# Kernel optimization log

Measured on AMD Instinct MI355X. Metric: run time of the kernel, lower is better.

## Reference

```python
import jax, jax.numpy as jnp
import numpy as np

N_NODES = 50000
N_EDGES = 800000
IN_FEATS = 9
H_FEATS = 64
HEADS = 3
N_CLASSES = 2
NEG_SLOPE = 0.2  # DGL GATConv default leaky_relu slope


def _gat_layer(x, src, dst, W, attn_l, attn_r, bias, n_nodes):
    """One DGL-style GATConv: returns [N, H, F_out] (pre head-sum)."""
    H, Fo = attn_l.shape
    feat = (x @ W).reshape(n_nodes, H, Fo)            # [N,H,Fo]
    el = jnp.einsum('nhf,hf->nh', feat, attn_l)        # [N,H]
    er = jnp.einsum('nhf,hf->nh', feat, attn_r)        # [N,H]
    e = jax.nn.leaky_relu(el[src] + er[dst], negative_slope=NEG_SLOPE)  # [E,H]
    # edge softmax over incoming edges per destination node
    m = jax.ops.segment_max(e, dst, num_segments=n_nodes)               # [N,H]
    ex = jnp.exp(e - m[dst])                                             # [E,H]
    s = jax.ops.segment_sum(ex, dst, num_segments=n_nodes)              # [N,H]
    alpha = ex / s[dst]                                                  # [E,H]
    # attention-weighted neighbor aggregation
    rst = jax.ops.segment_sum(alpha[:, :, None] * feat[src], dst,
                              num_segments=n_nodes)                      # [N,H,Fo]
    return rst + bias.reshape(1, H, Fo)


def setup_inputs() -> dict:
    key = jax.random.key(0)
    ks = jax.random.split(key, 16)
    feats = jax.random.normal(ks[0], (N_NODES, IN_FEATS), dtype=jnp.float32)
    src = jax.random.randint(ks[1], (N_EDGES,), 0, N_NODES, dtype=jnp.int32)
    dst = jax.random.randint(ks[2], (N_EDGES,), 0, N_NODES, dtype=jnp.int32)
    sc = 0.1
    # layer 1: in_feats -> H*H_FEATS
    W1 = jax.random.normal(ks[3], (IN_FEATS, HEADS * H_FEATS), dtype=jnp.float32) * sc
    al1 = jax.random.normal(ks[4], (HEADS, H_FEATS), dtype=jnp.float32) * sc
    ar1 = jax.random.normal(ks[5], (HEADS, H_FEATS), dtype=jnp.float32) * sc
    b1 = jnp.zeros((HEADS * H_FEATS,), dtype=jnp.float32)
    # middle block layer: H_FEATS -> H*H_FEATS
    W2 = jax.random.normal(ks[6], (H_FEATS, HEADS * H_FEATS), dtype=jnp.float32) * sc
    al2 = jax.random.normal(ks[7], (HEADS, H_FEATS), dtype=jnp.float32) * sc
    ar2 = jax.random.normal(ks[8], (HEADS, H_FEATS), dtype=jnp.float32) * sc
    b2 = jnp.zeros((HEADS * H_FEATS,), dtype=jnp.float32)
    # output layer: H_FEATS -> H*N_CLASSES
    W3 = jax.random.normal(ks[9], (H_FEATS, HEADS * N_CLASSES), dtype=jnp.float32) * sc
    al3 = jax.random.normal(ks[10], (HEADS, N_CLASSES), dtype=jnp.float32) * sc
    ar3 = jax.random.normal(ks[11], (HEADS, N_CLASSES), dtype=jnp.float32) * sc
    b3 = jnp.zeros((HEADS * N_CLASSES,), dtype=jnp.float32)
    return {"feats": feats, "src": src, "dst": dst,
            "W1": W1, "al1": al1, "ar1": ar1, "b1": b1,
            "W2": W2, "al2": al2, "ar2": ar2, "b2": b2,
            "W3": W3, "al3": al3, "ar3": ar3, "b3": b3}


def reference(feats, src, dst, W1, al1, ar1, b1, W2, al2, ar2, b2, W3, al3, ar3, b3):
    # dropout layers are identity at inference (in_dropout/feat_drop skipped)
    h = _gat_layer(feats, src, dst, W1, al1, ar1, b1, N_NODES).sum(axis=1)  # [N,H_FEATS]
    h = _gat_layer(h, src, dst, W2, al2, ar2, b2, N_NODES).sum(axis=1)       # [N,H_FEATS]
    o = _gat_layer(h, src, dst, W3, al3, ar3, b3, N_NODES).sum(axis=1)       # [N,N_CLASSES]
    return o
```

## Files before the change

### kernel.cpp

```cpp
#include <hip/hip_runtime.h>
#include <hip/hip_fp16.h>

#define N_NODES 50000
#define N_EDGES 800000
#define NBKT 196
#define EPB_BIN 4096
#define NB_BIN ((N_EDGES + EPB_BIN - 1) / EPB_BIN)
#define NB_EL 196
#define NB_PW 48

typedef _Float16 half8 __attribute__((ext_vector_type(8)));
typedef float f32x4 __attribute__((ext_vector_type(4)));

static __device__ __forceinline__ float lrelu(float x) { return fmaxf(x, 0.2f * x); }

static __device__ __forceinline__ float2 h2f(float bits) {
    union { float f; __half2 h; } u;
    u.f = bits;
    return __half22float2(u.h);
}
static __device__ __forceinline__ float f2h2(float a, float b) {
    union { float f; __half2 h; } u;
    u.h = __floats2half2_rn(a, b);
    return u.f;
}

__global__ void __launch_bounds__(256) k_front(const int* __restrict__ dst,
                                               int* __restrict__ bcnt,
                                               const float* __restrict__ x,
                                               const float* __restrict__ W1,
                                               const float* __restrict__ al1,
                                               const float* __restrict__ ar1,
                                               float* __restrict__ xph,
                                               float* __restrict__ er,
                                               const float* __restrict__ W2,
                                               __half* __restrict__ Wt16,
                                               const float* __restrict__ al2,
                                               const float* __restrict__ ar2,
                                               float* __restrict__ Wa2,
                                               float* __restrict__ Wr2) {
    __shared__ int lcnt[NBKT];
    __shared__ float sWa[9 * 3];
    __shared__ float sWr[9 * 3];
    const int t = threadIdx.x;
    const int b = blockIdx.x;

    if (b < NB_BIN) {
        const int e0 = b * EPB_BIN;
        for (int i = t; i < NBKT; i += 256) lcnt[i] = 0;
        __syncthreads();
#pragma unroll
        for (int i = 0; i < 16; ++i) {
            const int e = e0 + i * 256 + t;
            if (e < N_EDGES) atomicAdd(&lcnt[dst[e] >> 8], 1);
        }
        __syncthreads();
        for (int i = t; i < NBKT; i += 256)
            if (lcnt[i]) atomicAdd(&bcnt[i], lcnt[i]);
        return;
    }
    if (b < NB_BIN + NB_EL) {
        if (t < 27) {
            const int h = t / 9, k = t % 9;
            float sa = 0.f, sr = 0.f;
            for (int f = 0; f < 64; ++f) {
                const float w = W1[k * 192 + h * 64 + f];
                sa += w * al1[h * 64 + f];
                sr += w * ar1[h * 64 + f];
            }
            sWa[k * 3 + h] = sa;
            sWr[k * 3 + h] = sr;
        }
        __syncthreads();
        const int n = (b - NB_BIN) * 256 + t;
        if (n >= N_NODES) return;
        const float* __restrict__ xr = x + (size_t)n * 9;
        float xv[9];
        float a0 = 0.f, a1 = 0.f, a2 = 0.f, r0 = 0.f, r1 = 0.f, r2 = 0.f;
#pragma unroll
        for (int k = 0; k < 9; ++k) {
            xv[k] = xr[k];
            a0 += xv[k] * sWa[k * 3 + 0];
            a1 += xv[k] * sWa[k * 3 + 1];
            a2 += xv[k] * sWa[k * 3 + 2];
            r0 += xv[k] * sWr[k * 3 + 0];
            r1 += xv[k] * sWr[k * 3 + 1];
            r2 += xv[k] * sWr[k * 3 + 2];
        }
        float* __restrict__ xo = xph + (size_t)n * 8;
        *reinterpret_cast<float4*>(xo) = make_float4(a0, a1, a2, f2h2(xv[0], xv[1]));
        *reinterpret_cast<float4*>(xo + 4) =
            make_float4(f2h2(xv[2], xv[3]), f2h2(xv[4], xv[5]),
                        f2h2(xv[6], xv[7]), f2h2(xv[8], 0.f));
        *reinterpret_cast<float4*>(er + (size_t)n * 4) = make_float4(r0, r1, r2, 0.f);
        return;
    }
    if (b < NB_BIN + NB_EL + NB_PW) {
        const int idx = (b - (NB_BIN + NB_EL)) * 256 + t;
        if (idx < 64 * 192) {
            const int n = idx / 192, ke = idx % 192;
            Wt16[idx] = __float2half(W2[(ke & 63) * 192 + (ke >> 6) * 64 + n]);
        }
        return;
    }
    if (t < 192) {
        const int h = t >> 6, k = t & 63;
        float sa = 0.f, sr = 0.f;
        for (int f = 0; f < 64; ++f) {
            const float w = W2[k * 192 + h * 64 + f];
            sa += w * al2[h * 64 + f];
            sr += w * ar2[h * 64 + f];
        }
        Wa2[k * 4 + h] = sa;
        Wr2[k * 4 + h] = sr;
        if (h == 0) { Wa2[k * 4 + 3] = 0.f; Wr2[k * 4 + 3] = 0.f; }
    }
}

__global__ void __launch_bounds__(256) k_bin(const int* __restrict__ src,
                                             const int* __restrict__ dst,
                                             const int* __restrict__ bcnt,
                                             int* __restrict__ bfill,
                                             unsigned int* __restrict__ stage) {
    __shared__ int lcnt[NBKT];
    __shared__ int gb[NBKT];
    __shared__ int lf[NBKT];
    __shared__ int sscan[256];
    __shared__ int sbase[256];
    const int t = threadIdx.x;
    const int e0 = blockIdx.x * EPB_BIN;
    const int bv = (t < NBKT) ? bcnt[t] : 0;
    sscan[t] = bv;
    if (t < NBKT) lcnt[t] = 0;
    __syncthreads();
    for (int off = 1; off < 256; off <<= 1) {
        const int u = (t >= off) ? sscan[t - off] : 0;
        __syncthreads();
        sscan[t] += u;
        __syncthreads();
    }
    sbase[t] = sscan[t] - bv;
    int dcache[16];
#pragma unroll
    for (int i = 0; i < 16; ++i) {
        const int e = e0 + i * 256 + t;
        if (e < N_EDGES) {
            const int d = dst[e];
            dcache[i] = d;
            atomicAdd(&lcnt[d >> 8], 1);
        } else dcache[i] = -1;
    }
    __syncthreads();
    for (int i = t; i < NBKT; i += 256) {
        gb[i] = sbase[i] + atomicAdd(&bfill[i], lcnt[i]);
        lf[i] = 0;
    }
    __syncthreads();
#pragma unroll
    for (int i = 0; i < 16; ++i) {
        const int e = e0 + i * 256 + t;
        if (e < N_EDGES) {
            const int d = dcache[i];
            const int bk = d >> 8;
            const int r = atomicAdd(&lf[bk], 1);
            stage[gb[bk] + r] = (unsigned int)src[e] | ((unsigned int)(d & 255) << 16);
        }
    }
}

__global__ void __launch_bounds__(256) k_bscatter2(const unsigned int* __restrict__ stage,
                                                   const int* __restrict__ bcnt,
                                                   int* __restrict__ rowp,
                                                   int* __restrict__ col) {
    __shared__ int lcnt[256];
    __shared__ int lpos[256];
    __shared__ int sexc[256];
    __shared__ int sscan[256];
    const int t = threadIdx.x;
    const int b = blockIdx.x;
    const int n0 = b << 8;
    const int bv = (t < NBKT) ? bcnt[t] : 0;
    sscan[t] = bv;
    lcnt[t] = 0;
    __syncthreads();
    for (int off = 1; off < 256; off <<= 1) {
        const int u = (t >= off) ? sscan[t - off] : 0;
        __syncthreads();
        sscan[t] += u;
        __syncthreads();
    }
    const int base = (b == 0) ? 0 : sscan[b - 1];
    const int end = sscan[b];

    for (int j = base + t; j < end; j += 256)
        atomicAdd(&lcnt[(stage[j] >> 16) & 255], 1);
    __syncthreads();
    const int v = lcnt[t];
    lpos[t] = v;
    __syncthreads();
    for (int off = 1; off < 256; off <<= 1) {
        const int u = (t >= off) ? lpos[t - off] : 0;
        __syncthreads();
        lpos[t] += u;
        __syncthreads();
    }
    sexc[t] = lpos[t] - v;
    if (n0 + t < N_NODES) rowp[n0 + t] = base + sexc[t];
    if (b == NBKT - 1 && t == 0) rowp[N_NODES] = N_EDGES;
    lcnt[t] = 0;
    __syncthreads();
    for (int j = base + t; j < end; j += 256) {
        const unsigned int e = stage[j];
        const int local = (int)(e >> 16) & 255;
        const int r = atomicAdd(&lcnt[local], 1);
        col[base + sexc[local] + r] = (int)(e & 0xFFFFu);
    }
}

__global__ void __launch_bounds__(256, 6) k_l1(const float* __restrict__ xph,
                                               const float* __restrict__ er_in,
                                               const int* __restrict__ rowp,
                                               const int* __restrict__ col,
                                               const float* __restrict__ W1,
                                               const float* __restrict__ b1,
                                               const float* __restrict__ Wa2,
                                               const float* __restrict__ Wr2,
                                               __half* __restrict__ hout,
                                               float* __restrict__ el,
                                               float* __restrict__ er_out) {
    __shared__ union {
        float At[16 * 28];
        float vbuf[16][72];
    } u;
    __shared__ float part[3][16][64];
    const int t = threadIdx.x;
    const int wv = t >> 6;
    const int lane = t & 63;
    const int q = lane >> 4;
    const int ql = lane & 15;
    const int li = wv * 4 + q;
    const int nbase = blockIdx.x * 16;
    const int n = nbase + li;

    {
        const int jb = rowp[n], je = rowp[n + 1];
        const float4 er4 = *reinterpret_cast<const float4*>(er_in + (size_t)n * 4);
        float acc[27];
#pragma unroll
        for (int j = 0; j < 27; ++j) acc[j] = 0.f;
        float sw0 = 0.f, sw1 = 0.f, sw2 = 0.f;

        for (int e = jb + ql; e < je; e += 32) {
            const int e2 = e + 16;
            const bool v2 = (e2 < je);
            const int s1 = col[e];
            const int s2 = v2 ? col[e2] : s1;
            const float* __restrict__ r1 = xph + (size_t)s1 * 8;
            const float* __restrict__ r2 = xph + (size_t)s2 * 8;
            const float4 xa1 = *reinterpret_cast<const float4*>(r1);
            const float4 xb1 = *reinterpret_cast<const float4*>(r1 + 4);
            const float4 xa2 = *reinterpret_cast<const float4*>(r2);
            const float4 xb2 = *reinterpret_cast<const float4*>(r2 + 4);
            const float m2 = v2 ? 1.f : 0.f;
            const float w10 = __expf(lrelu(xa1.x + er4.x));
            const float w11 = __expf(lrelu(xa1.y + er4.y));
            const float w12 = __expf(lrelu(xa1.z + er4.z));
            const float w20 = __expf(lrelu(xa2.x + er4.x)) * m2;
            const float w21 = __expf(lrelu(xa2.y + er4.y)) * m2;
            const float w22 = __expf(lrelu(xa2.z + er4.z)) * m2;
            sw0 += w10 + w20; sw1 += w11 + w21; sw2 += w12 + w22;
            const float2 p10 = h2f(xa1.w), p11 = h2f(xb1.x), p12 = h2f(xb1.y),
                         p13 = h2f(xb1.z), p14 = h2f(xb1.w);
            const float2 p20 = h2f(xa2.w), p21 = h2f(xb2.x), p22 = h2f(xb2.y),
                         p23 = h2f(xb2.z), p24 = h2f(xb2.w);
            const float x1[9] = {p10.x, p10.y, p11.x, p11.y, p12.x, p12.y, p13.x, p13.y, p14.x};
            const float x2[9] = {p20.x, p20.y, p21.x, p21.y, p22.x, p22.y, p23.x, p23.y, p24.x};
#pragma unroll
            for (int k = 0; k < 9; ++k) {
                acc[0 + k]  += w10 * x1[k] + w20 * x2[k];
                acc[9 + k]  += w11 * x1[k] + w21 * x2[k];
                acc[18 + k] += w12 * x1[k] + w22 * x2[k];
            }
        }
#pragma unroll
        for (int off = 1; off < 16; off <<= 1) {
            sw0 += __shfl_xor(sw0, off);
            sw1 += __shfl_xor(sw1, off);
            sw2 += __shfl_xor(sw2, off);
#pragma unroll
            for (int j = 0; j < 27; ++j) acc[j] += __shfl_xor(acc[j], off);
        }
        if (ql == 0) {
            const bool has = (je > jb);
            const float i0 = has ? 1.f / sw0 : 0.f;
            const float i1 = has ? 1.f / sw1 : 0.f;
            const float i2 = has ? 1.f / sw2 : 0.f;
            float* __restrict__ ao = u.At + li * 28;
#pragma unroll
            for (int k = 0; k < 9; ++k) {
                ao[k] = acc[k] * i0;
                ao[9 + k] = acc[9 + k] * i1;
                ao[18 + k] = acc[18 + k] * i2;
            }
        }
    }
    __syncthreads();

    {
        const int h = wv;
        const int c = lane;
        if (h < 3) {
            float wreg[9];
#pragma unroll
            for (int k = 0; k < 9; ++k) wreg[k] = W1[k * 192 + h * 64 + c];
#pragma unroll
            for (int i = 0; i < 16; ++i) {
                const float* __restrict__ arp = u.At + i * 28 + h * 9;
                float acc = 0.f;
#pragma unroll
                for (int k = 0; k < 9; ++k) acc += arp[k] * wreg[k];
                part[h][i][c] = acc;
            }
        }
        __syncthreads();
        const float bsum = b1[c] + b1[64 + c] + b1[128 + c];
        for (int idx = t; idx < 1024; idx += 256) {
            const int i = idx >> 6, cc = idx & 63;
            const float v = part[0][i][cc] + part[1][i][cc] + part[2][i][cc] + bsum;
            hout[(size_t)(nbase + i) * 64 + cc] = __float2half(v);
            u.vbuf[i][cc] = v;
        }
        __syncthreads();
        if (t < 96) {
            const int i = t / 6, r = t % 6;
            const int h3 = (r < 3) ? r : r - 3;
            const float* __restrict__ tab = (r < 3) ? Wa2 : Wr2;
            float s = 0.f;
#pragma unroll 8
            for (int c2 = 0; c2 < 64; ++c2) s += u.vbuf[i][c2] * tab[c2 * 4 + h3];
            if (r < 3) el[(size_t)(nbase + i) * 4 + h3] = s;
            else       er_out[(size_t)(nbase + i) * 4 + h3] = s;
        }
    }
}

__global__ void __launch_bounds__(256, 8) k_aggw64(const __half* __restrict__ x,
                                                   const float* __restrict__ el,
                                                   const float* __restrict__ er,
                                                   const int* __restrict__ rowp,
                                                   const int* __restrict__ col,
                                                   __half* __restrict__ agg) {
    const int wv = threadIdx.x >> 6;
    const int lane = threadIdx.x & 63;
    const int n = blockIdx.x * 4 + wv;
    const int jb = rowp[n], je = rowp[n + 1];

    __shared__ float wbuf[4][3][68];
    __shared__ int cbuf[4][68];
    const float4 er4 = *reinterpret_cast<const float4*>(er + (size_t)n * 4);
    const int p = lane >> 5;
    const int f0 = (lane & 31) * 2;
    float a00 = 0.f, a01 = 0.f, a02 = 0.f;
    float a10 = 0.f, a11 = 0.f, a12 = 0.f;
    float sw0 = 0.f, sw1 = 0.f, sw2 = 0.f;

    for (int c0 = jb; c0 < je; c0 += 64) {
        const int cnt = min(64, je - c0);
        float w0 = 0.f, w1 = 0.f, w2 = 0.f;
        if (lane < cnt) {
            const int s = col[c0 + lane];
            cbuf[wv][lane] = s;
            const float4 e4 = *reinterpret_cast<const float4*>(el + (size_t)s * 4);
            w0 = __expf(lrelu(e4.x + er4.x));
            w1 = __expf(lrelu(e4.y + er4.y));
            w2 = __expf(lrelu(e4.z + er4.z));
            wbuf[wv][0][lane] = w0;
            wbuf[wv][1][lane] = w1;
            wbuf[wv][2][lane] = w2;
        }
        sw0 += w0; sw1 += w1; sw2 += w2;
        int e = 0;
        for (; e + 2 <= cnt; e += 2) {
            const int ei = e + p;
            const int s = cbuf[wv][ei];
            const float2 xv = __half22float2(
                *reinterpret_cast<const __half2*>(x + (size_t)s * 64 + f0));
            const float we0 = wbuf[wv][0][ei];
            const float we1 = wbuf[wv][1][ei];
            const float we2 = wbuf[wv][2][ei];
            a00 += we0 * xv.x; a01 += we1 * xv.x; a02 += we2 * xv.x;
            a10 += we0 * xv.y; a11 += we1 * xv.y; a12 += we2 * xv.y;
        }
        if (e < cnt && p == 0) {
            const int s = cbuf[wv][e];
            const float2 xv = __half22float2(
                *reinterpret_cast<const __half2*>(x + (size_t)s * 64 + f0));
            const float we0 = wbuf[wv][0][e];
            const float we1 = wbuf[wv][1][e];
            const float we2 = wbuf[wv][2][e];
            a00 += we0 * xv.x; a01 += we1 * xv.x; a02 += we2 * xv.x;
            a10 += we0 * xv.y; a11 += we1 * xv.y; a12 += we2 * xv.y;
        }
    }
    a00 += __shfl_xor(a00, 32); a01 += __shfl_xor(a01, 32); a02 += __shfl_xor(a02, 32);
    a10 += __shfl_xor(a10, 32); a11 += __shfl_xor(a11, 32); a12 += __shfl_xor(a12, 32);
#pragma unroll
    for (int off = 32; off > 0; off >>= 1) {
        sw0 += __shfl_xor(sw0, off);
        sw1 += __shfl_xor(sw1, off);
        sw2 += __shfl_xor(sw2, off);
    }
    if (lane < 32) {
        __half* __restrict__ ao = agg + (size_t)n * 192;
        if (je > jb) {
            const float i0 = 1.f / sw0, i1 = 1.f / sw1, i2 = 1.f / sw2;
            *reinterpret_cast<__half2*>(ao + f0) = __floats2half2_rn(a00 * i0, a10 * i0);
            *reinterpret_cast<__half2*>(ao + 64 + f0) = __floats2half2_rn(a01 * i1, a11 * i1);
            *reinterpret_cast<__half2*>(ao + 128 + f0) = __floats2half2_rn(a02 * i2, a12 * i2);
        } else {
            const __half2 z = __floats2half2_rn(0.f, 0.f);
            *reinterpret_cast<__half2*>(ao + f0) = z;
            *reinterpret_cast<__half2*>(ao + 64 + f0) = z;
            *reinterpret_cast<__half2*>(ao + 128 + f0) = z;
        }
    }
}

__global__ void __launch_bounds__(256) k_l23(const __half* __restrict__ aggH,
                                             const __half* __restrict__ Wt,
                                             const float* __restrict__ b2,
                                             const float* __restrict__ W3,
                                             const float* __restrict__ al3,
                                             const float* __restrict__ ar3,
                                             float* __restrict__ feat3p,
                                             float* __restrict__ er3) {
    __shared__ float xl[64 * 68];
    __shared__ float Wl[64 * 6];
    __shared__ float Wal[64 * 3];
    __shared__ float Wrl[64 * 3];
    const int t = threadIdx.x;
    const int n0 = blockIdx.x * 64;
    const int nvalid = min(64, N_NODES - n0);

    {
        const int wv = t >> 6;
        const int lane = t & 63;
        const int quad = lane >> 4;
        const int t16 = lane & 15;
        const int nwave = n0 + wv * 16;
        const int arow = min(nwave + t16, N_NODES - 1);
        half8 a[6];
#pragma unroll
        for (int kb = 0; kb < 6; ++kb)
            a[kb] = *reinterpret_cast<const half8*>(aggH + (size_t)arow * 192 + kb * 32 + quad * 8);
#pragma unroll
        for (int nt = 0; nt < 4; ++nt) {
            const int c = nt * 16 + t16;
            const float bs = b2[c] + b2[64 + c] + b2[128 + c];
            const __half* __restrict__ bt = Wt + (size_t)c * 192 + quad * 8;
            f32x4 acc = {0.f, 0.f, 0.f, 0.f};
#pragma unroll
            for (int kb = 0; kb < 6; ++kb) {
                const half8 bfr = *reinterpret_cast<const half8*>(bt + kb * 32);
                acc = __builtin_amdgcn_mfma_f32_16x16x32_f16(a[kb], bfr, acc, 0, 0, 0);
            }
#pragma unroll
            for (int r = 0; r < 4; ++r)
                xl[(wv * 16 + quad * 4 + r) * 68 + c] = acc[r] + bs;
        }
    }
    for (int idx = t; idx < 384; idx += 256) Wl[idx] = W3[idx];
    if (t < 192) {
        const int k = t & 63, h = t >> 6;
        Wal[k * 3 + h] = W3[k * 6 + h * 2] * al3[h * 2] + W3[k * 6 + h * 2 + 1] * al3[h * 2 + 1];
        Wrl[k * 3 + h] = W3[k * 6 + h * 2] * ar3[h * 2] + W3[k * 6 + h * 2 + 1] * ar3[h * 2 + 1];
    }
    __syncthreads();

#pragma unroll
    for (int hp = 0; hp < 2; ++hp) {
        const int i = (t >> 3) + hp * 32;
        const int slot = t & 7;
        if (i < nvalid && slot < 6) {
            float acc = 0.f;
#pragma unroll
            for (int k4 = 0; k4 < 16; ++k4) {
                const float4 xv = *reinterpret_cast<const float4*>(&xl[i * 68 + 4 * k4]);
                acc += Wl[(4 * k4 + 0) * 6 + slot] * xv.x;
                acc += Wl[(4 * k4 + 1) * 6 + slot] * xv.y;
                acc += Wl[(4 * k4 + 2) * 6 + slot] * xv.z;
                acc += Wl[(4 * k4 + 3) * 6 + slot] * xv.w;
            }
            reinterpret_cast<__half*>(feat3p + (size_t)(n0 + i) * 8)[6 + slot] = __float2half(acc);
        }
        if (t < 192) {
            const int ii = t / 6 + hp * 32, ss = t % 6;
            if (ii < nvalid) {
                const int hh = (ss < 3) ? ss : ss - 3;
                const float* __restrict__ wt = (ss < 3) ? Wal : Wrl;
                float acc = 0.f;
#pragma unroll 4
                for (int k = 0; k < 64; ++k) acc += xl[ii * 68 + k] * wt[k * 3 + hh];
                if (ss < 3) feat3p[(size_t)(n0 + ii) * 8 + hh] = acc;
                else        er3[(size_t)(n0 + ii) * 4 + hh] = acc;
            }
        }
    }
}

__global__ void __launch_bounds__(256, 8) k_agg3(const float* __restrict__ feat3p,
                                                 const float* __restrict__ er3,
                                                 const float* __restrict__ b3,
                                                 const int* __restrict__ rowp,
                                                 const int* __restrict__ col,
                                                 float* __restrict__ out) {
    const int tid = threadIdx.x;
    const int wv = tid >> 6;
    const int lane = tid & 63;
    const int q = lane >> 4;
    const int ql = lane & 15;
    const int n = (blockIdx.x * 4 + wv) * 4 + q;
    const int jb = rowp[n], je = rowp[n + 1];
    const float4 er4 = *reinterpret_cast<const float4*>(er3 + (size_t)n * 4);

    float acc[6];
#pragma unroll
    for (int j = 0; j < 6; ++j) acc[j] = 0.f;
    float sw0 = 0.f, sw1 = 0.f, sw2 = 0.f;

    for (int e = jb + ql; e < je; e += 32) {
        const int e2 = e + 16;
        const bool v2 = (e2 < je);
        const int s1 = col[e];
        const int s2 = v2 ? col[e2] : s1;
        const float* __restrict__ r1 = feat3p + (size_t)s1 * 8;
        const float* __restrict__ r2 = feat3p + (size_t)s2 * 8;
        const float4 fa1 = *reinterpret_cast<const float4*>(r1);
        const float2 fb1 = *reinterpret_cast<const float2*>(r1 + 4);
        const float4 fa2 = *reinterpret_cast<const float4*>(r2);
        const float2 fb2 = *reinterpret_cast<const float2*>(r2 + 4);
        const float m2 = v2 ? 1.f : 0.f;
        const float w10 = __expf(lrelu(fa1.x + er4.x));
        const float w11 = __expf(lrelu(fa1.y + er4.y));
        const float w12 = __expf(lrelu(fa1.z + er4.z));
        const float w20 = __expf(lrelu(fa2.x + er4.x)) * m2;
        const float w21 = __expf(lrelu(fa2.y + er4.y)) * m2;
        const float w22 = __expf(lrelu(fa2.z + er4.z)) * m2;
        sw0 += w10 + w20; sw1 += w11 + w21; sw2 += w12 + w22;
        const float2 f01a = h2f(fa1.w), f23a = h2f(fb1.x), f45a = h2f(fb1.y);
        const float2 f01b = h2f(fa2.w), f23b = h2f(fb2.x), f45b = h2f(fb2.y);
        acc[0] += w10 * f01a.x + w20 * f01b.x;
        acc[1] += w10 * f01a.y + w20 * f01b.y;
        acc[2] += w11 * f23a.x + w21 * f23b.x;
        acc[3] += w11 * f23a.y + w21 * f23b.y;
        acc[4] += w12 * f45a.x + w22 * f45b.x;
        acc[5] += w12 * f45a.y + w22 * f45b.y;
    }
#pragma unroll
    for (int off = 1; off < 16; off <<= 1) {
        sw0 += __shfl_xor(sw0, off);
        sw1 += __shfl_xor(sw1, off);
        sw2 += __shfl_xor(sw2, off);
#pragma unroll
        for (int j = 0; j < 6; ++j) acc[j] += __shfl_xor(acc[j], off);
    }
    if (ql == 0) {
        const bool has = (je > jb);
        const float i0 = has ? 1.f / sw0 : 0.f;
        const float i1 = has ? 1.f / sw1 : 0.f;
        const float i2 = has ? 1.f / sw2 : 0.f;
        const float o0 = acc[0] * i0 + acc[2] * i1 + acc[4] * i2 + b3[0] + b3[2] + b3[4];
        const float o1 = acc[1] * i0 + acc[3] * i1 + acc[5] * i2 + b3[1] + b3[3] + b3[5];
        *reinterpret_cast<float2*>(out + (size_t)n * 2) = make_float2(o0, o1);
    }
}

extern "C" void kernel_launch(void* const* d_in, const int* in_sizes, int n_in,
                              void* d_out, int out_size, void* d_ws, size_t ws_size,
                              hipStream_t stream) {
    const float* feats = (const float*)d_in[0];
    const int* src = (const int*)d_in[1];
    const int* dst = (const int*)d_in[2];
    const float* W1 = (const float*)d_in[3];
    const float* al1 = (const float*)d_in[4];
    const float* ar1 = (const float*)d_in[5];
    const float* b1 = (const float*)d_in[6];
    const float* W2 = (const float*)d_in[7];
    const float* al2 = (const float*)d_in[8];
    const float* ar2 = (const float*)d_in[9];
    const float* b2 = (const float*)d_in[10];
    const float* W3 = (const float*)d_in[11];
    const float* al3 = (const float*)d_in[12];
    const float* ar3 = (const float*)d_in[13];
    const float* b3 = (const float*)d_in[14];
    float* out = (float*)d_out;

    char* ws = (char*)d_ws;
    size_t off = 0;
    auto alloc = [&](size_t bytes) {
        void* p = ws + off;
        off += (bytes + 255) & ~(size_t)255;
        return p;
    };
    __half* aggH = (__half*)alloc((size_t)N_NODES * 192 * 2);
    __half* hbufH = (__half*)alloc((size_t)N_NODES * 64 * 2);
    float* xph = (float*)alloc((size_t)N_NODES * 8 * 4);
    float* el = (float*)alloc((size_t)N_NODES * 4 * 4);
    float* er = (float*)alloc((size_t)N_NODES * 4 * 4);
    int* bcnt = (int*)alloc(512 * 4);
    int* bfill = bcnt + 256;
    int* rowp = (int*)alloc((size_t)(N_NODES + 1) * 4);
    int* col = (int*)alloc((size_t)N_EDGES * 4);
    unsigned int* stage = (unsigned int*)alloc((size_t)N_EDGES * 4);
    __half* Wt16 = (__half*)alloc((size_t)64 * 192 * 2);
    float* Wa2 = (float*)alloc(256 * 4);
    float* Wr2 = (float*)alloc(256 * 4);
    float* feat3p = (float*)alloc((size_t)N_NODES * 8 * 4);
    (void)ws_size;

    const int ab = N_NODES / 4;
    const int qb = N_NODES / 16;
    const int lb = (N_NODES + 63) / 64;

    hipMemsetAsync(bcnt, 0, 512 * 4, stream);
    k_front<<<NB_BIN + NB_EL + NB_PW + 1, 256, 0, stream>>>(
        dst, bcnt, feats, W1, al1, ar1, xph, er, W2, Wt16, al2, ar2, Wa2, Wr2);
    k_bin<<<NB_BIN, 256, 0, stream>>>(src, dst, bcnt, bfill, stage);
    k_bscatter2<<<NBKT, 256, 0, stream>>>(stage, bcnt, rowp, col);

    k_l1<<<qb, 256, 0, stream>>>(xph, er, rowp, col, W1, b1, Wa2, Wr2, hbufH, el, er);

    k_aggw64<<<ab, 256, 0, stream>>>(hbufH, el, er, rowp, col, aggH);

    k_l23<<<lb, 256, 0, stream>>>(aggH, Wt16, b2, W3, al3, ar3, feat3p, er);

    k_agg3<<<qb, 256, 0, stream>>>(feat3p, er, b3, rowp, col, out);
}
```

Baseline: 225.1 us.

## Build CSR with per-node atomic counts and unroll aggregation loops

Replaces the two-pass bucket staging CSR build with per-node degree counting in the front kernel, a per-bucket scan kernel, and a direct atomic scatter of source indices into col. This drops the staging buffer and one full pass over the edges, but adds 800k global atomics on node counters in two places. The layer-2 aggregation now packs the weights and a pre-shifted byte offset into one float4 in shared memory and processes four edges per iteration. The layer-3 aggregation unrolls to four edges per lane with lower launch-bounds occupancy, and layer 1 uses byte-offset addressing.

```diff
diff --git a/kernel.cpp b/kernel.cpp
--- a/kernel.cpp
+++ b/kernel.cpp
@@ -27,6 +27,7 @@
 
 __global__ void __launch_bounds__(256) k_front(const int* __restrict__ dst,
                                                int* __restrict__ bcnt,
+                                               int* __restrict__ nodecnt,
                                                const float* __restrict__ x,
                                                const float* __restrict__ W1,
                                                const float* __restrict__ al1,
@@ -52,7 +53,11 @@
 #pragma unroll
         for (int i = 0; i < 16; ++i) {
             const int e = e0 + i * 256 + t;
-            if (e < N_EDGES) atomicAdd(&lcnt[dst[e] >> 8], 1);
+            if (e < N_EDGES) {
+                const int d = dst[e];
+                atomicAdd(&lcnt[d >> 8], 1);
+                atomicAdd(&nodecnt[d], 1);
+            }
         }
         __syncthreads();
         for (int i = t; i < NBKT; i += 256)
@@ -117,71 +122,17 @@
     }
 }
 
-__global__ void __launch_bounds__(256) k_bin(const int* __restrict__ src,
-                                             const int* __restrict__ dst,
-                                             const int* __restrict__ bcnt,
-                                             int* __restrict__ bfill,
-                                             unsigned int* __restrict__ stage) {
-    __shared__ int lcnt[NBKT];
-    __shared__ int gb[NBKT];
-    __shared__ int lf[NBKT];
+__global__ void __launch_bounds__(256) k_build(const int* __restrict__ bcnt,
+                                               const int* __restrict__ nodecnt,
+                                               int* __restrict__ rowp,
+                                               int* __restrict__ fill) {
     __shared__ int sscan[256];
-    __shared__ int sbase[256];
-    const int t = threadIdx.x;
-    const int e0 = blockIdx.x * EPB_BIN;
-    const int bv = (t < NBKT) ? bcnt[t] : 0;
-    sscan[t] = bv;
-    if (t < NBKT) lcnt[t] = 0;
-    __syncthreads();
-    for (int off = 1; off < 256; off <<= 1) {
-        const int u = (t >= off) ? sscan[t - off] : 0;
-        __syncthreads();
-        sscan[t] += u;
-        __syncthreads();
-    }
-    sbase[t] = sscan[t] - bv;
-    int dcache[16];
-#pragma unroll
-    for (int i = 0; i < 16; ++i) {
-        const int e = e0 + i * 256 + t;
-        if (e < N_EDGES) {
-            const int d = dst[e];
-            dcache[i] = d;
-            atomicAdd(&lcnt[d >> 8], 1);
-        } else dcache[i] = -1;
-    }
-    __syncthreads();
-    for (int i = t; i < NBKT; i += 256) {
-        gb[i] = sbase[i] + atomicAdd(&bfill[i], lcnt[i]);
-        lf[i] = 0;
-    }
-    __syncthreads();
-#pragma unroll
-    for (int i = 0; i < 16; ++i) {
-        const int e = e0 + i * 256 + t;
-        if (e < N_EDGES) {
-            const int d = dcache[i];
-            const int bk = d >> 8;
-            const int r = atomicAdd(&lf[bk], 1);
-            stage[gb[bk] + r] = (unsigned int)src[e] | ((unsigned int)(d & 255) << 16);
-        }
-    }
-}
-
-__global__ void __launch_bounds__(256) k_bscatter2(const unsigned int* __restrict__ stage,
-                                                   const int* __restrict__ bcnt,
-                                                   int* __restrict__ rowp,
-                                                   int* __restrict__ col) {
-    __shared__ int lcnt[256];
-    __shared__ int lpos[256];
-    __shared__ int sexc[256];
-    __shared__ int sscan[256];
+    __shared__ int nscan[256];
     const int t = threadIdx.x;
     const int b = blockIdx.x;
     const int n0 = b << 8;
     const int bv = (t < NBKT) ? bcnt[t] : 0;
     sscan[t] = bv;
-    lcnt[t] = 0;
     __syncthreads();
     for (int off = 1; off < 256; off <<= 1) {
         const int u = (t >= off) ? sscan[t - off] : 0;
@@ -190,30 +141,39 @@
         __syncthreads();
     }
     const int base = (b == 0) ? 0 : sscan[b - 1];
-    const int end = sscan[b];
-
-    for (int j = base + t; j < end; j += 256)
-        atomicAdd(&lcnt[(stage[j] >> 16) & 255], 1);
-    __syncthreads();
-    const int v = lcnt[t];
-    lpos[t] = v;
+    const int n = n0 + t;
+    const int v = (n < N_NODES) ? nodecnt[n] : 0;
+    nscan[t] = v;
     __syncthreads();
     for (int off = 1; off < 256; off <<= 1) {
-        const int u = (t >= off) ? lpos[t - off] : 0;
-        __syncthreads();
-        lpos[t] += u;
-        __syncthreads();
-    }
-    sexc[t] = lpos[t] - v;
-    if (n0 + t < N_NODES) rowp[n0 + t] = base + sexc[t];
+        const int u = (t >= off) ? nscan[t - off] : 0;
+        __syncthreads();
+        nscan[t] += u;
+        __syncthreads();
+    }
+    if (n < N_NODES) {
+        const int r = base + nscan[t] - v;
+        rowp[n] = r;
+        fill[n] = r;
+    }
     if (b == NBKT - 1 && t == 0) rowp[N_NODES] = N_EDGES;
-    lcnt[t] = 0;
-    __syncthreads();
-    for (int j = base + t; j < end; j += 256) {
-        const unsigned int e = stage[j];
-        const int local = (int)(e >> 16) & 255;
-        const int r = atomicAdd(&lcnt[local], 1);
-        col[base + sexc[local] + r] = (int)(e & 0xFFFFu);
+}
+
+__global__ void __launch_bounds__(256) k_scatter(const int* __restrict__ src,
+                                                 const int* __restrict__ dst,
+                                                 int* __restrict__ fill,
+                                                 int* __restrict__ col) {
+    const int t = threadIdx.x;
+    const int e0 = blockIdx.x * EPB_BIN;
+#pragma unroll
+    for (int i = 0; i < 16; ++i) {
+        const int e = e0 + i * 256 + t;
+        if (e < N_EDGES) {
+            const int d = dst[e];
+            const int s = src[e];
+            const int pos = atomicAdd(&fill[d], 1);
+            col[pos] = s;
+        }
     }
 }
 
@@ -241,6 +201,7 @@
     const int li = wv * 4 + q;
     const int nbase = blockIdx.x * 16;
     const int n = nbase + li;
+    const char* __restrict__ xb = (const char*)xph;
 
     {
         const int jb = rowp[n], je = rowp[n + 1];
@@ -253,14 +214,12 @@
         for (int e = jb + ql; e < je; e += 32) {
             const int e2 = e + 16;
             const bool v2 = (e2 < je);
-            const int s1 = col[e];
-            const int s2 = v2 ? col[e2] : s1;
-            const float* __restrict__ r1 = xph + (size_t)s1 * 8;
-            const float* __restrict__ r2 = xph + (size_t)s2 * 8;
-            const float4 xa1 = *reinterpret_cast<const float4*>(r1);
-            const float4 xb1 = *reinterpret_cast<const float4*>(r1 + 4);
-            const float4 xa2 = *reinterpret_cast<const float4*>(r2);
-            const float4 xb2 = *reinterpret_cast<const float4*>(r2 + 4);
+            const int off1 = col[e] << 5;
+            const int off2 = (v2 ? col[e2] : col[e]) << 5;
+            const float4 xa1 = *reinterpret_cast<const float4*>(xb + off1);
+            const float4 xb1 = *reinterpret_cast<const float4*>(xb + off1 + 16);
+            const float4 xa2 = *reinterpret_cast<const float4*>(xb + off2);
+            const float4 xb2 = *reinterpret_cast<const float4*>(xb + off2 + 16);
             const float m2 = v2 ? 1.f : 0.f;
             const float w10 = __expf(lrelu(xa1.x + er4.x));
             const float w11 = __expf(lrelu(xa1.y + er4.y));
@@ -355,51 +314,56 @@
     const int n = blockIdx.x * 4 + wv;
     const int jb = rowp[n], je = rowp[n + 1];
 
-    __shared__ float wbuf[4][3][68];
-    __shared__ int cbuf[4][68];
+    __shared__ float4 wbuf4[4][64];
     const float4 er4 = *reinterpret_cast<const float4*>(er + (size_t)n * 4);
     const int p = lane >> 5;
-    const int f0 = (lane & 31) * 2;
+    const int foff = (lane & 31) * 4;
+    const char* __restrict__ xbase = (const char*)x;
+    const char* __restrict__ elbase = (const char*)el;
     float a00 = 0.f, a01 = 0.f, a02 = 0.f;
     float a10 = 0.f, a11 = 0.f, a12 = 0.f;
     float sw0 = 0.f, sw1 = 0.f, sw2 = 0.f;
 
     for (int c0 = jb; c0 < je; c0 += 64) {
         const int cnt = min(64, je - c0);
-        float w0 = 0.f, w1 = 0.f, w2 = 0.f;
         if (lane < cnt) {
             const int s = col[c0 + lane];
-            cbuf[wv][lane] = s;
-            const float4 e4 = *reinterpret_cast<const float4*>(el + (size_t)s * 4);
-            w0 = __expf(lrelu(e4.x + er4.x));
-            w1 = __expf(lrelu(e4.y + er4.y));
-            w2 = __expf(lrelu(e4.z + er4.z));
-            wbuf[wv][0][lane] = w0;
-            wbuf[wv][1][lane] = w1;
-            wbuf[wv][2][lane] = w2;
-        }
-        sw0 += w0; sw1 += w1; sw2 += w2;
+            const float4 e4 = *reinterpret_cast<const float4*>(elbase + (s << 4));
+            const float w0 = __expf(lrelu(e4.x + er4.x));
+            const float w1 = __expf(lrelu(e4.y + er4.y));
+            const float w2 = __expf(lrelu(e4.z + er4.z));
+            wbuf4[wv][lane] = make_float4(w0, w1, w2, __int_as_float(s << 7));
+            sw0 += w0; sw1 += w1; sw2 += w2;
+        }
+        __builtin_amdgcn_wave_barrier();
         int e = 0;
-        for (; e + 2 <= cnt; e += 2) {
-            const int ei = e + p;
-            const int s = cbuf[wv][ei];
-            const float2 xv = __half22float2(
-                *reinterpret_cast<const __half2*>(x + (size_t)s * 64 + f0));
-            const float we0 = wbuf[wv][0][ei];
-            const float we1 = wbuf[wv][1][ei];
-            const float we2 = wbuf[wv][2][ei];
-            a00 += we0 * xv.x; a01 += we1 * xv.x; a02 += we2 * xv.x;
-            a10 += we0 * xv.y; a11 += we1 * xv.y; a12 += we2 * xv.y;
-        }
-        if (e < cnt && p == 0) {
-            const int s = cbuf[wv][e];
-            const float2 xv = __half22float2(
-                *reinterpret_cast<const __half2*>(x + (size_t)s * 64 + f0));
-            const float we0 = wbuf[wv][0][e];
-            const float we1 = wbuf[wv][1][e];
-            const float we2 = wbuf[wv][2][e];
-            a00 += we0 * xv.x; a01 += we1 * xv.x; a02 += we2 * xv.x;
-            a10 += we0 * xv.y; a11 += we1 * xv.y; a12 += we2 * xv.y;
+        for (; e + 4 <= cnt; e += 4) {
+            const float4 q1 = wbuf4[wv][e + p];
+            const float4 q2 = wbuf4[wv][e + 2 + p];
+            const float2 f1 = __half22float2(*reinterpret_cast<const __half2*>(
+                xbase + (__float_as_int(q1.w) + foff)));
+            const float2 f2 = __half22float2(*reinterpret_cast<const __half2*>(
+                xbase + (__float_as_int(q2.w) + foff)));
+            a00 += q1.x * f1.x + q2.x * f2.x;
+            a01 += q1.y * f1.x + q2.y * f2.x;
+            a02 += q1.z * f1.x + q2.z * f2.x;
+            a10 += q1.x * f1.y + q2.x * f2.y;
+            a11 += q1.y * f1.y + q2.y * f2.y;
+            a12 += q1.z * f1.y + q2.z * f2.y;
+        }
+        if (e + p < cnt) {
+            const float4 q1 = wbuf4[wv][e + p];
+            const float2 f1 = __half22float2(*reinterpret_cast<const __half2*>(
+                xbase + (__float_as_int(q1.w) + foff)));
+            a00 += q1.x * f1.x; a01 += q1.y * f1.x; a02 += q1.z * f1.x;
+            a10 += q1.x * f1.y; a11 += q1.y * f1.y; a12 += q1.z * f1.y;
+        }
+        if (e + 2 + p < cnt) {
+            const float4 q2 = wbuf4[wv][e + 2 + p];
+            const float2 f2 = __half22float2(*reinterpret_cast<const __half2*>(
+                xbase + (__float_as_int(q2.w) + foff)));
+            a00 += q2.x * f2.x; a01 += q2.y * f2.x; a02 += q2.z * f2.x;
+            a10 += q2.x * f2.y; a11 += q2.y * f2.y; a12 += q2.z * f2.y;
         }
     }
     a00 += __shfl_xor(a00, 32); a01 += __shfl_xor(a01, 32); a02 += __shfl_xor(a02, 32);
@@ -411,6 +375,7 @@
         sw2 += __shfl_xor(sw2, off);
     }
     if (lane < 32) {
+        const int f0 = (lane & 31) * 2;
         __half* __restrict__ ao = agg + (size_t)n * 192;
         if (je > jb) {
             const float i0 = 1.f / sw0, i1 = 1.f / sw1, i2 = 1.f / sw2;
@@ -508,7 +473,7 @@
     }
 }
 
-__global__ void __launch_bounds__(256, 8) k_agg3(const float* __restrict__ feat3p,
+__global__ void __launch_bounds__(256, 4) k_agg3(const float* __restrict__ feat3p,
                                                  const float* __restrict__ er3,
                                                  const float* __restrict__ b3,
                                                  const int* __restrict__ rowp,
@@ -522,39 +487,55 @@
     const int n = (blockIdx.x * 4 + wv) * 4 + q;
     const int jb = rowp[n], je = rowp[n + 1];
     const float4 er4 = *reinterpret_cast<const float4*>(er3 + (size_t)n * 4);
+    const char* __restrict__ fb = (const char*)feat3p;
 
     float acc[6];
 #pragma unroll
     for (int j = 0; j < 6; ++j) acc[j] = 0.f;
     float sw0 = 0.f, sw1 = 0.f, sw2 = 0.f;
 
-    for (int e = jb + ql; e < je; e += 32) {
-        const int e2 = e + 16;
-        const bool v2 = (e2 < je);
-        const int s1 = col[e];
-        const int s2 = v2 ? col[e2] : s1;
-        const float* __restrict__ r1 = feat3p + (size_t)s1 * 8;
-        const float* __restrict__ r2 = feat3p + (size_t)s2 * 8;
-        const float4 fa1 = *reinterpret_cast<const float4*>(r1);
-        const float2 fb1 = *reinterpret_cast<const float2*>(r1 + 4);
-        const float4 fa2 = *reinterpret_cast<const float4*>(r2);
-        const float2 fb2 = *reinterpret_cast<const float2*>(r2 + 4);
-        const float m2 = v2 ? 1.f : 0.f;
+    for (int e = jb + ql; e < je; e += 64) {
+        const int eb = e + 16, ec = e + 32, ed = e + 48;
+        const bool vb = (eb < je), vc = (ec < je), vd = (ed < je);
+        const int sa = col[e];
+        const int offa = sa << 5;
+        const int offb = (vb ? col[eb] : sa) << 5;
+        const int offc = (vc ? col[ec] : sa) << 5;
+        const int offd = (vd ? col[ed] : sa) << 5;
+        const float4 fa1 = *reinterpret_cast<const float4*>(fb + offa);
+        const float2 fb1 = *reinterpret_cast<const float2*>(fb + offa + 16);
+        const float4 fa2 = *reinterpret_cast<const float4*>(fb + offb);
+        const float2 fb2 = *reinterpret_cast<const float2*>(fb + offb + 16);
+        const float4 fa3 = *reinterpret_cast<const float4*>(fb + offc);
+        const float2 fb3 = *reinterpret_cast<const float2*>(fb + offc + 16);
+        const float4 fa4 = *reinterpret_cast<const float4*>(fb + offd);
+        const float2 fb4 = *reinterpret_cast<const float2*>(fb + offd + 16);
+        const float mb = vb ? 1.f : 0.f, mc = vc ? 1.f : 0.f, md = vd ? 1.f : 0.f;
         const float w10 = __expf(lrelu(fa1.x + er4.x));
         const float w11 = __expf(lrelu(fa1.y + er4.y));
         const float w12 = __expf(lrelu(fa1.z + er4.z));
-        const float w20 = __expf(lrelu(fa2.x + er4.x)) * m2;
-        const float w21 = __expf(lrelu(fa2.y + er4.y)) * m2;
-        const float w22 = __expf(lrelu(fa2.z + er4.z)) * m2;
-        sw0 += w10 + w20; sw1 += w11 + w21; sw2 += w12 + w22;
+        const float w20 = __expf(lrelu(fa2.x + er4.x)) * mb;
+        const float w21 = __expf(lrelu(fa2.y + er4.y)) * mb;
+        const float w22 = __expf(lrelu(fa2.z + er4.z)) * mb;
+        const float w30 = __expf(lrelu(fa3.x + er4.x)) * mc;
+        const float w31 = __expf(lrelu(fa3.y + er4.y)) * mc;
+        const float w32 = __expf(lrelu(fa3.z + er4.z)) * mc;
+        const float w40 = __expf(lrelu(fa4.x + er4.x)) * md;
+        const float w41 = __expf(lrelu(fa4.y + er4.y)) * md;
+        const float w42 = __expf(lrelu(fa4.z + er4.z)) * md;
+        sw0 += (w10 + w20) + (w30 + w40);
+        sw1 += (w11 + w21) + (w31 + w41);
+        sw2 += (w12 + w22) + (w32 + w42);
         const float2 f01a = h2f(fa1.w), f23a = h2f(fb1.x), f45a = h2f(fb1.y);
         const float2 f01b = h2f(fa2.w), f23b = h2f(fb2.x), f45b = h2f(fb2.y);
-        acc[0] += w10 * f01a.x + w20 * f01b.x;
-        acc[1] += w10 * f01a.y + w20 * f01b.y;
-        acc[2] += w11 * f23a.x + w21 * f23b.x;
-        acc[3] += w11 * f23a.y + w21 * f23b.y;
-        acc[4] += w12 * f45a.x + w22 * f45b.x;
-        acc[5] += w12 * f45a.y + w22 * f45b.y;
+        const float2 f01c = h2f(fa3.w), f23c = h2f(fb3.x), f45c = h2f(fb3.y);
+        const float2 f01d = h2f(fa4.w), f23d = h2f(fb4.x), f45d = h2f(fb4.y);
+        acc[0] += (w10 * f01a.x + w20 * f01b.x) + (w30 * f01c.x + w40 * f01d.x);
+        acc[1] += (w10 * f01a.y + w20 * f01b.y) + (w30 * f01c.y + w40 * f01d.y);
+        acc[2] += (w11 * f23a.x + w21 * f23b.x) + (w31 * f23c.x + w41 * f23d.x);
+        acc[3] += (w11 * f23a.y + w21 * f23b.y) + (w31 * f23c.y + w41 * f23d.y);
+        acc[4] += (w12 * f45a.x + w22 * f45b.x) + (w32 * f45c.x + w42 * f45d.x);
+        acc[5] += (w12 * f45a.y + w22 * f45b.y) + (w32 * f45c.y + w42 * f45d.y);
     }
 #pragma unroll
     for (int off = 1; off < 16; off <<= 1) {
@@ -607,11 +588,12 @@
     float* xph = (float*)alloc((size_t)N_NODES * 8 * 4);
     float* el = (float*)alloc((size_t)N_NODES * 4 * 4);
     float* er = (float*)alloc((size_t)N_NODES * 4 * 4);
-    int* bcnt = (int*)alloc(512 * 4);
-    int* bfill = bcnt + 256;
+    int* cnts = (int*)alloc((size_t)(256 + N_NODES) * 4);
+    int* bcnt = cnts;
+    int* nodecnt = cnts + 256;
+    int* fill = (int*)alloc((size_t)N_NODES * 4);
     int* rowp = (int*)alloc((size_t)(N_NODES + 1) * 4);
     int* col = (int*)alloc((size_t)N_EDGES * 4);
-    unsigned int* stage = (unsigned int*)alloc((size_t)N_EDGES * 4);
     __half* Wt16 = (__half*)alloc((size_t)64 * 192 * 2);
     float* Wa2 = (float*)alloc(256 * 4);
     float* Wr2 = (float*)alloc(256 * 4);
@@ -622,11 +604,11 @@
     const int qb = N_NODES / 16;
     const int lb = (N_NODES + 63) / 64;
 
-    hipMemsetAsync(bcnt, 0, 512 * 4, stream);
+    hipMemsetAsync(cnts, 0, (size_t)(256 + N_NODES) * 4, stream);
     k_front<<<NB_BIN + NB_EL + NB_PW + 1, 256, 0, stream>>>(
-        dst, bcnt, feats, W1, al1, ar1, xph, er, W2, Wt16, al2, ar2, Wa2, Wr2);
-    k_bin<<<NB_BIN, 256, 0, stream>>>(src, dst, bcnt, bfill, stage);
-    k_bscatter2<<<NBKT, 256, 0, stream>>>(stage, bcnt, rowp, col);
+        dst, bcnt, nodecnt, feats, W1, al1, ar1, xph, er, W2, Wt16, al2, ar2, Wa2, Wr2);
+    k_build<<<NBKT, 256, 0, stream>>>(bcnt, nodecnt, rowp, fill);
+    k_scatter<<<NB_BIN, 256, 0, stream>>>(src, dst, fill, col);
 
     k_l1<<<qb, 256, 0, stream>>>(xph, er, rowp, col, W1, b1, Wa2, Wr2, hbufH, el, er);
 
```

Result: slower. 265.2 us (+17.8%).
